# Performance work log

Measured on AMD Instinct MI355X. Metric: run time of the kernel, lower is better.

Reference implementation:

```python
import jax, jax.numpy as jnp
import numpy as np

NOT_EPSILON = 1.0

def swishmax(x, axis):
    # x * exp(x - max) normalized by sum(|.|) + 1 over `axis`
    xexp = x * jnp.exp(x - jnp.max(x, axis=axis, keepdims=True))
    return xexp / (jnp.sum(jnp.abs(xexp), axis=axis, keepdims=True) + NOT_EPSILON)

def setup_inputs() -> dict:
    key = jax.random.key(0)
    ks = jax.random.split(key, 8)
    B, S, D = 2, 512, 256
    std = 0.02
    x = jax.random.normal(ks[0], (B, S, D), dtype=jnp.float32)
    w_pre = jax.random.normal(ks[1], (D, D), dtype=jnp.float32) * std
    w_q   = jax.random.normal(ks[2], (D, D), dtype=jnp.float32) * std
    w_k   = jax.random.normal(ks[3], (D, D), dtype=jnp.float32) * std
    w_va  = jax.random.normal(ks[4], (D, D), dtype=jnp.float32) * std
    w_al  = jax.random.normal(ks[5], (D, D), dtype=jnp.float32) * std
    w_vo  = jax.random.normal(ks[6], (D, D), dtype=jnp.float32) * std
    w_end = jax.random.normal(ks[7], (D, D), dtype=jnp.float32) * std
    return {"x": x, "w_pre": w_pre, "w_q": w_q, "w_k": w_k,
            "w_va": w_va, "w_al": w_al, "w_vo": w_vo, "w_end": w_end}

def reference(x, w_pre, w_q, w_k, w_va, w_al, w_vo, w_end):
    # pre: module_1d = Linear(D, D, bias=False)
    X = x @ w_pre.T                                    # [B,S,D]
    # FractalAttention depth=2 (base case): row_dims=(-3,)
    q = X + X @ w_q.T                                  # residual query proj
    k = X + X @ w_k.T                                  # residual key proj
    # batchify: key lhs -> [B,Sk,1,D], query rhs -> [B,1,Sq,D]
    raw = k[:, :, None, :] * q[:, None, :, :]          # [B,Sk,Sq,D]
    logits = raw + raw @ w_al.T                        # residual logit proj over D
    scale = swishmax(logits, axis=-3)                  # normalize over Sk
    v = X + X @ w_va.T
    vs = v[:, :, None, :] * scale                      # [B,Sk,Sq,D]
    vsum = jnp.sum(vs, axis=-3)                        # [B,Sq,D]
    vout = vsum + vsum @ w_vo.T
    X = X + vout                                       # transformer residual
    X = X @ w_end.T                                    # end: module_1d
    return X
```

## Files before the change

kernel.cpp:

```cpp
#include <hip/hip_runtime.h>
#include <hip/hip_bf16.h>


typedef __attribute__((ext_vector_type(8))) short short8;
typedef __attribute__((ext_vector_type(4))) float f32x4;
typedef __attribute__((ext_vector_type(8))) _Float16 half8;
typedef __attribute__((ext_vector_type(4))) _Float16 half4;

#define DD 256
#define SS 512
#define LOG2E 1.4426950408889634f
#define LN2   0.6931471805599453f

__device__ __forceinline__ unsigned short f2bf(float f) {
  unsigned int b = __float_as_uint(f);
  b += 0x7FFFu + ((b >> 16) & 1u);
  return (unsigned short)(b >> 16);
}
__device__ __forceinline__ short8 cvt8(f32x4 lo, f32x4 hi) {
  short8 r;
  r[0]=(short)f2bf(lo[0]); r[1]=(short)f2bf(lo[1]);
  r[2]=(short)f2bf(lo[2]); r[3]=(short)f2bf(lo[3]);
  r[4]=(short)f2bf(hi[0]); r[5]=(short)f2bf(hi[1]);
  r[6]=(short)f2bf(hi[2]); r[7]=(short)f2bf(hi[3]);
  return r;
}

__global__ __launch_bounds__(256) void prep_weights(
    const float* __restrict__ w0, const float* __restrict__ w1,
    const float* __restrict__ w2, const float* __restrict__ w3,
    const float* __restrict__ w4, const float* __restrict__ w5,
    const float* __restrict__ wal, unsigned short* __restrict__ out)
{
  const int bi = blockIdx.x;
  const int m = bi >> 5;
  const int off = ((bi & 31) * 256 + threadIdx.x) * 8;
  const float* src = m==0?w0: m==1?w1: m==2?w2: m==3?w3: m==4?w4: m==5?w5: wal;
  f32x4 a = *(const f32x4*)(src + off);
  f32x4 b = *(const f32x4*)(src + off + 4);
  if (m == 6) {
    const int e = off >> 8, d = off & 255;
#pragma unroll
    for (int jj = 0; jj < 4; ++jj) {
      if (e == d + jj)     a[jj] += 1.0f;
      if (e == d + 4 + jj) b[jj] += 1.0f;
    }
    half8 h;
#pragma unroll
    for (int jj = 0; jj < 4; ++jj) {
      h[jj]     = (_Float16)a[jj];
      h[jj + 4] = (_Float16)b[jj];
    }
    *(half8*)(out + (size_t)m * 65536 + off) = h;
  } else {
    *(short8*)(out + (size_t)m * 65536 + off) = cvt8(a, b);
  }
}

__global__ __launch_bounds__(256) void linear_bf(
    const float* __restrict__ A, const unsigned short* __restrict__ Wbf,
    const float* __restrict__ res1, const float* __restrict__ res2,
    float* __restrict__ out)
{
  const int bi = blockIdx.x;
  const int rb = (bi >> 2) * 16;
  const int cb = (bi & 3) * 64;
  const int tid = threadIdx.x;
  const int wv = tid >> 6, lane = tid & 63;
  const int g = lane >> 4, c = lane & 15;
  const int arow = rb + c;
  const int wrow = cb + wv * 16 + c;

  f32x4 acc = (f32x4){0.f, 0.f, 0.f, 0.f};
#pragma unroll
  for (int ks = 0; ks < 8; ++ks) {
    const int d0 = ks * 32 + g * 8;
    f32x4 a0 = *(const f32x4*)(A + arow * DD + d0);
    f32x4 a1 = *(const f32x4*)(A + arow * DD + d0 + 4);
    short8 av = cvt8(a0, a1);
    short8 bv = *(const short8*)(Wbf + wrow * DD + d0);
    acc = __builtin_amdgcn_mfma_f32_16x16x32_bf16(av, bv, acc, 0, 0, 0);
  }
#pragma unroll
  for (int j = 0; j < 4; ++j) {
    const int ro = rb + g * 4 + j;
    const int co = cb + wv * 16 + c;
    float v = acc[j];
    if (res1) v += res1[ro * DD + co];
    if (res2) v += res2[ro * DD + co];
    out[ro * DD + co] = v;
  }
}

__global__ __launch_bounds__(256) void linear_qkv(
    const float* __restrict__ X,
    const unsigned short* __restrict__ Wq, const unsigned short* __restrict__ Wk,
    const unsigned short* __restrict__ Wv,
    _Float16* __restrict__ qout, _Float16* __restrict__ kout,
    _Float16* __restrict__ vout)
{
  const int bi = blockIdx.x;
  const int rb = (bi >> 2) * 16;
  const int cb = (bi & 3) * 64;
  const int tid = threadIdx.x;
  const int wv = tid >> 6, lane = tid & 63;
  const int g = lane >> 4, c = lane & 15;
  const int arow = rb + c;
  const int wrow = cb + wv * 16 + c;

  f32x4 aq = (f32x4){0.f,0.f,0.f,0.f};
  f32x4 ak = (f32x4){0.f,0.f,0.f,0.f};
  f32x4 av_ = (f32x4){0.f,0.f,0.f,0.f};
#pragma unroll
  for (int ks = 0; ks < 8; ++ks) {
    const int d0 = ks * 32 + g * 8;
    f32x4 a0 = *(const f32x4*)(X + arow * DD + d0);
    f32x4 a1 = *(const f32x4*)(X + arow * DD + d0 + 4);
    short8 af = cvt8(a0, a1);
    short8 bq = *(const short8*)(Wq + wrow * DD + d0);
    aq = __builtin_amdgcn_mfma_f32_16x16x32_bf16(af, bq, aq, 0, 0, 0);
    short8 bk = *(const short8*)(Wk + wrow * DD + d0);
    ak = __builtin_amdgcn_mfma_f32_16x16x32_bf16(af, bk, ak, 0, 0, 0);
    short8 bv = *(const short8*)(Wv + wrow * DD + d0);
    av_ = __builtin_amdgcn_mfma_f32_16x16x32_bf16(af, bv, av_, 0, 0, 0);
  }
#pragma unroll
  for (int j = 0; j < 4; ++j) {
    const int ro = rb + g * 4 + j;
    const int co = cb + wv * 16 + c;
    const float base = X[ro * DD + co];
    qout[ro * DD + co] = (_Float16)((base + aq[j]) * LOG2E);
    kout[ro * DD + co] = (_Float16)(base + ak[j]);
    vout[ro * DD + co] = (_Float16)(base + av_[j]);
  }
}

__global__ __launch_bounds__(256) void pack_kv(
    const _Float16* __restrict__ k, const _Float16* __restrict__ v,
    _Float16* __restrict__ kfrag, _Float16* __restrict__ vfrag)
{
  const int id = blockIdx.x * 256 + threadIdx.x;
  if (id < 32768) {
    const int lane = id & 63, ks = (id >> 6) & 7, t2 = (id >> 9) & 31, b = id >> 14;
    const int g = lane >> 4, c = lane & 15;
    const _Float16* src = k + ((size_t)(b * SS + t2 * 16 + c) * DD + ks * 32 + g * 8);
    *(half8*)(kfrag + (size_t)id * 8) = *(const half8*)src;
  } else {
    const int id2 = id - 32768;
    const int lane = id2 & 63, i = (id2 >> 6) & 3, wv = (id2 >> 8) & 3,
              t2 = (id2 >> 10) & 31, b = id2 >> 15;
    const int g = lane >> 4, c = lane & 15;
    const _Float16* src = v + ((size_t)(b * SS + t2 * 16 + c) * DD + wv * 64 + i * 16 + g * 4);
    *(half4*)(vfrag + (size_t)id2 * 4) = *(const half4*)src;
  }
}

__global__ __launch_bounds__(64, 2) void fractal_attn(
    const _Float16* __restrict__ walI,
    const _Float16* __restrict__ qf,
    const _Float16* __restrict__ kfrag,
    const _Float16* __restrict__ vfrag,
    float* __restrict__ vsum)
{
  const int bid = blockIdx.x;
  const int wv = bid & 3;
  const int sq = (bid >> 2) & 511;
  const int b  = bid >> 11;
  const int lane = threadIdx.x;
  const int g = lane >> 4, c = lane & 15;

  half8 afrag[4][8];
  {
    const _Float16* qrow = qf + (size_t)(b * SS + sq) * DD;
    half8 q8[8];
#pragma unroll
    for (int ks = 0; ks < 8; ++ks)
      q8[ks] = *(const half8*)(qrow + ks * 32 + g * 8);
#pragma unroll
    for (int i = 0; i < 4; ++i) {
      const int e = wv * 64 + i * 16 + c;
      const _Float16* wrow = walI + (size_t)e * DD;
#pragma unroll
      for (int ks = 0; ks < 8; ++ks)
        afrag[i][ks] = (*(const half8*)(wrow + ks * 32 + g * 8)) * q8[ks];
    }
  }

  const _Float16* kfb = kfrag + (size_t)b * 131072 + lane * 8;
  const _Float16* vfb = vfrag + (size_t)b * 131072 + wv * 1024 + lane * 4;

  float mst[16], sst[16], vst[16];
#pragma unroll
  for (int s = 0; s < 16; ++s) { mst[s] = -1e30f; sst[s] = 0.f; vst[s] = 0.f; }

  for (int t2 = 0; t2 < 32; ++t2) {
    const _Float16* kf = kfb + t2 * 4096;
    const _Float16* vf = vfb + t2 * 4096;

    half8 bf[8];
#pragma unroll
    for (int ks = 0; ks < 8; ++ks)
      bf[ks] = *(const half8*)(kf + ks * 512);
    half4 vvq[4];
#pragma unroll
    for (int i = 0; i < 4; ++i)
      vvq[i] = *(const half4*)(vf + i * 256);

    f32x4 acc[4];
    __builtin_amdgcn_s_setprio(1);
    {
      const f32x4 zeroc = (f32x4){0.f, 0.f, 0.f, 0.f};
#pragma unroll
      for (int i = 0; i < 4; ++i)
        acc[i] = __builtin_amdgcn_mfma_f32_16x16x32_f16(afrag[i][0], bf[0], zeroc, 0, 0, 0);
#pragma unroll
      for (int ks = 1; ks < 8; ++ks)
#pragma unroll
        for (int i = 0; i < 4; ++i)
          acc[i] = __builtin_amdgcn_mfma_f32_16x16x32_f16(afrag[i][ks], bf[ks], acc[i], 0, 0, 0);
    }
    __builtin_amdgcn_s_setprio(0);

#pragma unroll
    for (int i = 0; i < 4; ++i) {
#pragma unroll
      for (int j = 0; j < 4; ++j) {
        const int s = i * 4 + j;
        const float L = acc[i][j];
        mst[s] = fmaxf(mst[s], L);
        const float p = L * __builtin_amdgcn_exp2f(L);
        sst[s] += fabsf(p);
        vst[s] = fmaf((float)vvq[i][j], p, vst[s]);
      }
    }
  }

#pragma unroll
  for (int mask = 1; mask <= 8; mask <<= 1) {
#pragma unroll
    for (int s = 0; s < 16; ++s) {
      mst[s] = fmaxf(mst[s], __shfl_xor(mst[s], mask));
      sst[s] += __shfl_xor(sst[s], mask);
      vst[s] += __shfl_xor(vst[s], mask);
    }
  }

  if (c == 0) {
    float* orow = vsum + (size_t)(b * SS + sq) * DD;
#pragma unroll
    for (int i = 0; i < 4; ++i) {
      f32x4 o;
#pragma unroll
      for (int j = 0; j < 4; ++j) {
        const int s = i * 4 + j;
        const float tt = LN2 * __builtin_amdgcn_exp2f(-mst[s]);
        o[j] = vst[s] * tt / (sst[s] * tt + 1.0f);
      }
      *(f32x4*)(orow + wv * 64 + i * 16 + g * 4) = o;
    }
  }
}

extern "C" void kernel_launch(void* const* d_in, const int* in_sizes, int n_in,
                              void* d_out, int out_size, void* d_ws, size_t ws_size,
                              hipStream_t stream) {
  const float* x     = (const float*)d_in[0];
  const float* w_pre = (const float*)d_in[1];
  const float* w_q   = (const float*)d_in[2];
  const float* w_k   = (const float*)d_in[3];
  const float* w_va  = (const float*)d_in[4];
  const float* w_al  = (const float*)d_in[5];
  const float* w_vo  = (const float*)d_in[6];
  const float* w_end = (const float*)d_in[7];
  float* out = (float*)d_out;

  char* ws = (char*)d_ws;
  float*    X     = (float*)(ws);
  float*    Y     = (float*)(ws + (1 << 20));
  float*    vsum  = (float*)(ws + (2 << 20));
  _Float16* qf16  = (_Float16*)(ws + (3 << 20));
  _Float16* kf16  = (_Float16*)(ws + (3 << 20) + (512 << 10));
  _Float16* vf16  = (_Float16*)(ws + (4 << 20));
  _Float16* kfrag = (_Float16*)(ws + (4 << 20) + (512 << 10));
  _Float16* vfrag = (_Float16*)(ws + (5 << 20));
  unsigned short* wbf = (unsigned short*)(ws + (5 << 20) + (512 << 10));

  prep_weights<<<224, 256, 0, stream>>>(w_pre, w_q, w_k, w_va, w_vo, w_end,
                                        w_al, wbf);
  linear_bf<<<256, 256, 0, stream>>>(x, wbf + 0 * 65536, nullptr, nullptr, X);
  linear_qkv<<<256, 256, 0, stream>>>(X, wbf + 1 * 65536, wbf + 2 * 65536,
                                      wbf + 3 * 65536, qf16, kf16, vf16);
  pack_kv<<<384, 256, 0, stream>>>(kf16, vf16, kfrag, vfrag);
  fractal_attn<<<4096, 64, 0, stream>>>((const _Float16*)(wbf + 6 * 65536),
                                        qf16, kfrag, vfrag, vsum);
  linear_bf<<<256, 256, 0, stream>>>(vsum, wbf + 4 * 65536, vsum, X, Y);
  linear_bf<<<256, 256, 0, stream>>>(Y, wbf + 5 * 65536, nullptr, nullptr, out);
}
```

Baseline: 120.9 us.

## Merge four attention waves per block and software-pipeline MFMA with softmax updates

The attention kernel now runs the four D-slice waves of one query row as a single 256-thread block instead of four 64-thread blocks. Its Sk loop is double-buffered with two accumulator and V register sets, so the exp/accumulate update for one tile overlaps the MFMA chain and loads of the next. The aim is to hide MFMA and load latency behind the VALU update and to let the waves sharing K fragments sit on the same CU. The cost is higher register pressure from the duplicated accumulators under the launch_bounds(256,2) limit, which risks spills or lower occupancy.

```diff
diff --git a/kernel.cpp b/kernel.cpp
--- a/kernel.cpp
+++ b/kernel.cpp
@@ -155,7 +155,7 @@
   }
 }
 
-__global__ __launch_bounds__(64, 2) void fractal_attn(
+__global__ __launch_bounds__(256, 2) void fractal_attn(
     const _Float16* __restrict__ walI,
     const _Float16* __restrict__ qf,
     const _Float16* __restrict__ kfrag,
@@ -163,10 +163,11 @@
     float* __restrict__ vsum)
 {
   const int bid = blockIdx.x;
-  const int wv = bid & 3;
-  const int sq = (bid >> 2) & 511;
-  const int b  = bid >> 11;
-  const int lane = threadIdx.x;
+  const int sq = bid & 511;
+  const int b  = bid >> 9;
+  const int tid = threadIdx.x;
+  const int wv = tid >> 6;
+  const int lane = tid & 63;
   const int g = lane >> 4, c = lane & 15;
 
   half8 afrag[4][8];
@@ -193,47 +194,75 @@
 #pragma unroll
   for (int s = 0; s < 16; ++s) { mst[s] = -1e30f; sst[s] = 0.f; vst[s] = 0.f; }
 
-  for (int t2 = 0; t2 < 32; ++t2) {
-    const _Float16* kf = kfb + t2 * 4096;
-    const _Float16* vf = vfb + t2 * 4096;
-
-    half8 bf[8];
-#pragma unroll
-    for (int ks = 0; ks < 8; ++ks)
-      bf[ks] = *(const half8*)(kf + ks * 512);
-    half4 vvq[4];
-#pragma unroll
-    for (int i = 0; i < 4; ++i)
-      vvq[i] = *(const half4*)(vf + i * 256);
-
-    f32x4 acc[4];
-    __builtin_amdgcn_s_setprio(1);
-    {
-      const f32x4 zeroc = (f32x4){0.f, 0.f, 0.f, 0.f};
-#pragma unroll
-      for (int i = 0; i < 4; ++i)
-        acc[i] = __builtin_amdgcn_mfma_f32_16x16x32_f16(afrag[i][0], bf[0], zeroc, 0, 0, 0);
-#pragma unroll
-      for (int ks = 1; ks < 8; ++ks)
-#pragma unroll
-        for (int i = 0; i < 4; ++i)
-          acc[i] = __builtin_amdgcn_mfma_f32_16x16x32_f16(afrag[i][ks], bf[ks], acc[i], 0, 0, 0);
-    }
-    __builtin_amdgcn_s_setprio(0);
-
-#pragma unroll
-    for (int i = 0; i < 4; ++i) {
-#pragma unroll
-      for (int j = 0; j < 4; ++j) {
-        const int s = i * 4 + j;
-        const float L = acc[i][j];
-        mst[s] = fmaxf(mst[s], L);
-        const float p = L * __builtin_amdgcn_exp2f(L);
-        sst[s] += fabsf(p);
-        vst[s] = fmaf((float)vvq[i][j], p, vst[s]);
-      }
-    }
-  }
+  half8 bf[8];
+  half4 vqA[4], vqB[4];
+  f32x4 accA[4], accB[4];
+  const f32x4 zeroc = (f32x4){0.f, 0.f, 0.f, 0.f};
+
+#define LOADK(T2)                                                   \
+  {                                                                 \
+    const _Float16* kf_ = kfb + (T2) * 4096;                        \
+    _Pragma("unroll")                                               \
+    for (int ks = 0; ks < 8; ++ks)                                  \
+      bf[ks] = *(const half8*)(kf_ + ks * 512);                     \
+  }
+#define LOADV(T2, VQ)                                               \
+  {                                                                 \
+    const _Float16* vf_ = vfb + (T2) * 4096;                        \
+    _Pragma("unroll")                                               \
+    for (int i = 0; i < 4; ++i)                                     \
+      VQ[i] = *(const half4*)(vf_ + i * 256);                       \
+  }
+#define MFMA_INTO(ACC)                                              \
+  {                                                                 \
+    __builtin_amdgcn_s_setprio(1);                                  \
+    _Pragma("unroll")                                               \
+    for (int i = 0; i < 4; ++i)                                     \
+      ACC[i] = __builtin_amdgcn_mfma_f32_16x16x32_f16(              \
+          afrag[i][0], bf[0], zeroc, 0, 0, 0);                      \
+    _Pragma("unroll")                                               \
+    for (int ks = 1; ks < 8; ++ks)                                  \
+      _Pragma("unroll")                                             \
+      for (int i = 0; i < 4; ++i)                                   \
+        ACC[i] = __builtin_amdgcn_mfma_f32_16x16x32_f16(            \
+            afrag[i][ks], bf[ks], ACC[i], 0, 0, 0);                 \
+    __builtin_amdgcn_s_setprio(0);                                  \
+  }
+#define UPDATE(ACC, VQ)                                             \
+  {                                                                 \
+    _Pragma("unroll")                                               \
+    for (int i = 0; i < 4; ++i)                                     \
+      _Pragma("unroll")                                             \
+      for (int j = 0; j < 4; ++j) {                                 \
+        const int s = i * 4 + j;                                    \
+        const float L = ACC[i][j];                                  \
+        mst[s] = fmaxf(mst[s], L);                                  \
+        const float p = L * __builtin_amdgcn_exp2f(L);              \
+        sst[s] += fabsf(p);                                         \
+        vst[s] = fmaf((float)VQ[i][j], p, vst[s]);                  \
+      }                                                             \
+  }
+
+  LOADK(0); LOADV(0, vqA);
+  MFMA_INTO(accA);
+#pragma unroll 1
+  for (int t2 = 1; t2 < 31; t2 += 2) {
+    LOADK(t2); LOADV(t2, vqB);
+    UPDATE(accA, vqA);
+    MFMA_INTO(accB);
+    LOADK(t2 + 1); LOADV(t2 + 1, vqA);
+    UPDATE(accB, vqB);
+    MFMA_INTO(accA);
+  }
+  LOADK(31); LOADV(31, vqB);
+  UPDATE(accA, vqA);
+  MFMA_INTO(accB);
+  UPDATE(accB, vqB);
+
+#undef LOADK
+#undef LOADV
+#undef MFMA_INTO
+#undef UPDATE
 
 #pragma unroll
   for (int mask = 1; mask <= 8; mask <<= 1) {
@@ -291,8 +320,8 @@
   linear_qkv<<<256, 256, 0, stream>>>(X, wbf + 1 * 65536, wbf + 2 * 65536,
                                       wbf + 3 * 65536, qf16, kf16, vf16);
   pack_kv<<<384, 256, 0, stream>>>(kf16, vf16, kfrag, vfrag);
-  fractal_attn<<<4096, 64, 0, stream>>>((const _Float16*)(wbf + 6 * 65536),
-                                        qf16, kfrag, vfrag, vsum);
+  fractal_attn<<<1024, 256, 0, stream>>>((const _Float16*)(wbf + 6 * 65536),
+                                         qf16, kfrag, vfrag, vsum);
   linear_bf<<<256, 256, 0, stream>>>(vsum, wbf + 4 * 65536, vsum, X, Y);
   linear_bf<<<256, 256, 0, stream>>>(Y, wbf + 5 * 65536, nullptr, nullptr, out);
 }
```

After: 273.4 us. 126% more time.

## Merge four attention waves per block and software-pipeline K/V fragment loads

Applied to the files above, without the earlier changes.

The attention kernel now launches one 256-thread block per query row, with four waves each covering a 64-wide D slice, instead of one 64-thread block per wave. The K and V fragment loads for the next key tile are issued right after the current MFMA chain and after the softmax update, so their latency overlaps compute. A per-iteration s_barrier keeps the waves in lockstep so they share K fragments in cache. The cost is an extra barrier every iteration, and more live registers for the in-flight fragments, which may reduce occupancy.

```diff
diff --git a/kernel.cpp b/kernel.cpp
--- a/kernel.cpp
+++ b/kernel.cpp
@@ -155,7 +155,7 @@
   }
 }
 
-__global__ __launch_bounds__(64, 2) void fractal_attn(
+__global__ __launch_bounds__(256, 2) void fractal_attn(
     const _Float16* __restrict__ walI,
     const _Float16* __restrict__ qf,
     const _Float16* __restrict__ kfrag,
@@ -163,10 +163,11 @@
     float* __restrict__ vsum)
 {
   const int bid = blockIdx.x;
-  const int wv = bid & 3;
-  const int sq = (bid >> 2) & 511;
-  const int b  = bid >> 11;
-  const int lane = threadIdx.x;
+  const int sq = bid & 511;
+  const int b  = bid >> 9;
+  const int tid = threadIdx.x;
+  const int wv = tid >> 6;
+  const int lane = tid & 63;
   const int g = lane >> 4, c = lane & 15;
 
   half8 afrag[4][8];
@@ -193,33 +194,36 @@
 #pragma unroll
   for (int s = 0; s < 16; ++s) { mst[s] = -1e30f; sst[s] = 0.f; vst[s] = 0.f; }
 
+  half8 bf[8];
+  half4 vq[4];
+  f32x4 acc[4];
+  const f32x4 zeroc = (f32x4){0.f, 0.f, 0.f, 0.f};
+
+#pragma unroll
+  for (int ks = 0; ks < 8; ++ks) bf[ks] = *(const half8*)(kfb + ks * 512);
+#pragma unroll
+  for (int i = 0; i < 4; ++i) vq[i] = *(const half4*)(vfb + i * 256);
+
+#pragma unroll 1
   for (int t2 = 0; t2 < 32; ++t2) {
-    const _Float16* kf = kfb + t2 * 4096;
-    const _Float16* vf = vfb + t2 * 4096;
-
-    half8 bf[8];
-#pragma unroll
-    for (int ks = 0; ks < 8; ++ks)
-      bf[ks] = *(const half8*)(kf + ks * 512);
-    half4 vvq[4];
+    __builtin_amdgcn_s_barrier();
+
+    __builtin_amdgcn_s_setprio(1);
 #pragma unroll
     for (int i = 0; i < 4; ++i)
-      vvq[i] = *(const half4*)(vf + i * 256);
-
-    f32x4 acc[4];
-    __builtin_amdgcn_s_setprio(1);
-    {
-      const f32x4 zeroc = (f32x4){0.f, 0.f, 0.f, 0.f};
+      acc[i] = __builtin_amdgcn_mfma_f32_16x16x32_f16(afrag[i][0], bf[0], zeroc, 0, 0, 0);
+#pragma unroll
+    for (int ks = 1; ks < 8; ++ks)
 #pragma unroll
       for (int i = 0; i < 4; ++i)
-        acc[i] = __builtin_amdgcn_mfma_f32_16x16x32_f16(afrag[i][0], bf[0], zeroc, 0, 0, 0);
-#pragma unroll
-      for (int ks = 1; ks < 8; ++ks)
-#pragma unroll
-        for (int i = 0; i < 4; ++i)
-          acc[i] = __builtin_amdgcn_mfma_f32_16x16x32_f16(afrag[i][ks], bf[ks], acc[i], 0, 0, 0);
-    }
+        acc[i] = __builtin_amdgcn_mfma_f32_16x16x32_f16(afrag[i][ks], bf[ks], acc[i], 0, 0, 0);
     __builtin_amdgcn_s_setprio(0);
+
+    if (t2 < 31) {
+      const _Float16* kf_ = kfb + (t2 + 1) * 4096;
+#pragma unroll
+      for (int ks = 0; ks < 8; ++ks) bf[ks] = *(const half8*)(kf_ + ks * 512);
+    }
 
 #pragma unroll
     for (int i = 0; i < 4; ++i) {
@@ -230,8 +234,14 @@
         mst[s] = fmaxf(mst[s], L);
         const float p = L * __builtin_amdgcn_exp2f(L);
         sst[s] += fabsf(p);
-        vst[s] = fmaf((float)vvq[i][j], p, vst[s]);
+        vst[s] = fmaf((float)vq[i][j], p, vst[s]);
       }
+    }
+
+    if (t2 < 31) {
+      const _Float16* vf_ = vfb + (t2 + 1) * 4096;
+#pragma unroll
+      for (int i = 0; i < 4; ++i) vq[i] = *(const half4*)(vf_ + i * 256);
     }
   }
 
@@ -291,8 +301,8 @@
   linear_qkv<<<256, 256, 0, stream>>>(X, wbf + 1 * 65536, wbf + 2 * 65536,
                                       wbf + 3 * 65536, qf16, kf16, vf16);
   pack_kv<<<384, 256, 0, stream>>>(kf16, vf16, kfrag, vfrag);
-  fractal_attn<<<4096, 64, 0, stream>>>((const _Float16*)(wbf + 6 * 65536),
-                                        qf16, kfrag, vfrag, vsum);
+  fractal_attn<<<1024, 256, 0, stream>>>((const _Float16*)(wbf + 6 * 65536),
+                                         qf16, kfrag, vfrag, vsum);
   linear_bf<<<256, 256, 0, stream>>>(vsum, wbf + 4 * 65536, vsum, X, Y);
   linear_bf<<<256, 256, 0, stream>>>(Y, wbf + 5 * 65536, nullptr, nullptr, out);
 }
```

New measurement: 123.7 us. +2.3%, slower.
